# Performance work log

Hardware: AMD Instinct MI355X
Metric: run time of the kernel (lower is better)

The kernel has to match this reference:

```python
import jax, jax.numpy as jnp
import numpy as np

D = 2048      # d_hidden
F = 1408      # d_expert (routed)
E = 8         # n_routed_experts
K = 2         # n_experts_per_token
FS = 2816     # shared expert width = d_expert * n_shared_experts
B, S = 2, 1024


def setup_inputs() -> dict:
    key = jax.random.key(0)
    ks = jax.random.split(key, 9)
    sc = 0.02
    return {
        "x": jax.random.normal(ks[0], (B, S, D), dtype=jnp.float32),
        "Wr": jax.random.normal(ks[1], (E, D), dtype=jnp.float32) * sc,   # router Linear(d_hidden, E).weight
        "Wg": jax.random.normal(ks[2], (E, F, D), dtype=jnp.float32) * sc,  # per-expert W_gate.weight [F,D]
        "Wu": jax.random.normal(ks[3], (E, F, D), dtype=jnp.float32) * sc,  # per-expert W_up.weight
        "Wd": jax.random.normal(ks[4], (E, D, F), dtype=jnp.float32) * sc,  # per-expert W_down.weight [D,F]
        "Wsg": jax.random.normal(ks[5], (FS, D), dtype=jnp.float32) * sc,   # shared expert W_gate
        "Wsu": jax.random.normal(ks[6], (FS, D), dtype=jnp.float32) * sc,   # shared expert W_up
        "Wsd": jax.random.normal(ks[7], (D, FS), dtype=jnp.float32) * sc,   # shared expert W_down
    }


def reference(x, Wr, Wg, Wu, Wd, Wsg, Wsu, Wsd):
    silu = jax.nn.silu

    # Shared expert: SwiGLU FFN over all tokens
    sg = silu(jnp.einsum("bsd,fd->bsf", x, Wsg))
    su = jnp.einsum("bsd,fd->bsf", x, Wsu)
    shared_out = jnp.einsum("bsf,df->bsd", sg * su, Wsd)

    # Gating: softmax over expert logits, then top-k (sum-combine is order-invariant)
    logits = jnp.einsum("bsd,ed->bse", x, Wr)
    scores = jax.nn.softmax(logits, axis=-1)
    topk_scores, topk_idx = jax.lax.top_k(scores, K)            # [B,S,K]
    # Dense combine weights [B,S,E]: topk score where selected, else 0
    w_full = jnp.sum(jax.nn.one_hot(topk_idx, E, dtype=x.dtype) * topk_scores[..., None], axis=-2)

    # Routed experts (dense-over-experts equivalent of sorted grouped-GEMM dispatch)
    g = silu(jnp.einsum("bsd,efd->bsef", x, Wg))                # [B,S,E,F]
    u = jnp.einsum("bsd,efd->bsef", x, Wu)
    out_e = jnp.einsum("bsef,edf->bsed", g * u, Wd)             # [B,S,E,D]
    routed_out = jnp.einsum("bsed,bse->bsd", out_e, w_full)

    return routed_out + shared_out
```

## Files before the change

kernel.cpp:

```cpp
#include <hip/hip_runtime.h>
#include <hip/hip_bf16.h>

#define D_HID 2048
#define F_EXP 1408
#define E_NUM 8
#define FS_SH 2816
#define T_TOK 2048

#define O_WSG 0
#define O_WSU 5767168
#define O_WG  11534336
#define O_WU  34603008
#define O_WSD 57671680
#define O_WD  63438848
#define W_TOT 86507520

#define MAXT 24
#define GU_SH_BLK 176
#define DN_SH_BLK 128

typedef __attribute__((ext_vector_type(8))) short bf16x8;
typedef __attribute__((ext_vector_type(4))) float f32x4;
typedef __attribute__((ext_vector_type(4))) unsigned short u16x4;

#define AS1 __attribute__((address_space(1)))
#define AS3 __attribute__((address_space(3)))

__device__ __forceinline__ unsigned short f2bf(float f){
  unsigned u = __float_as_uint(f);
  u += 0x7fffu + ((u >> 16) & 1u);
  return (unsigned short)(u >> 16);
}

__global__ void convert_x_kernel(const float* __restrict__ x, unsigned short* __restrict__ xb){
  const int i = blockIdx.x * blockDim.x + threadIdx.x;
  float4 v = ((const float4*)x)[i];
  u16x4 h;
  h[0]=f2bf(v.x); h[1]=f2bf(v.y); h[2]=f2bf(v.z); h[3]=f2bf(v.w);
  ((u16x4*)xb)[i] = h;
}

__global__ __launch_bounds__(256) void convert_w_kernel(
    const float* __restrict__ Wsg, const float* __restrict__ Wsu,
    const float* __restrict__ Wg,  const float* __restrict__ Wu,
    const float* __restrict__ Wsd, const float* __restrict__ Wd,
    unsigned short* __restrict__ dst)
{
  const long e0 = ((long)blockIdx.x * 256 + threadIdx.x) * 8;
  const float* src; long lo;
  if      (e0 < (long)O_WSU){ src = Wsg; lo = e0 - O_WSG; }
  else if (e0 < (long)O_WG ){ src = Wsu; lo = e0 - O_WSU; }
  else if (e0 < (long)O_WU ){ src = Wg;  lo = e0 - O_WG;  }
  else if (e0 < (long)O_WSD){ src = Wu;  lo = e0 - O_WU;  }
  else if (e0 < (long)O_WD ){ src = Wsd; lo = e0 - O_WSD; }
  else                      { src = Wd;  lo = e0 - O_WD;  }
  const float4 a = ((const float4*)(src + lo))[0];
  const float4 b = ((const float4*)(src + lo))[1];
  u16x4 h0, h1;
  h0[0]=f2bf(a.x); h0[1]=f2bf(a.y); h0[2]=f2bf(a.z); h0[3]=f2bf(a.w);
  h1[0]=f2bf(b.x); h1[1]=f2bf(b.y); h1[2]=f2bf(b.z); h1[3]=f2bf(b.w);
  ((u16x4*)(dst + e0))[0] = h0;
  ((u16x4*)(dst + e0))[1] = h1;
}

__global__ __launch_bounds__(64) void router_kernel(const float* __restrict__ x,
                                                    const float* __restrict__ Wr,
                                                    int* __restrict__ topk_e,
                                                    float* __restrict__ topk_w){
  const int t = blockIdx.x;
  const int lane = threadIdx.x;
  const float* xt = x + (size_t)t * D_HID;
  float acc[E_NUM];
  #pragma unroll
  for (int e=0;e<E_NUM;e++) acc[e]=0.f;
  for (int d=lane; d<D_HID; d+=64){
    const float xv = xt[d];
    #pragma unroll
    for (int e=0;e<E_NUM;e++) acc[e] += xv * Wr[e*D_HID + d];
  }
  #pragma unroll
  for (int e=0;e<E_NUM;e++){
    #pragma unroll
    for (int off=32; off>0; off>>=1) acc[e] += __shfl_xor(acc[e], off);
  }
  if (lane==0){
    float m = acc[0];
    #pragma unroll
    for (int e=1;e<E_NUM;e++) m = fmaxf(m, acc[e]);
    float p[E_NUM]; float s = 0.f;
    #pragma unroll
    for (int e=0;e<E_NUM;e++){ p[e] = expf(acc[e]-m); s += p[e]; }
    const float inv = 1.f/s;
    int i0=0; float b0=p[0];
    #pragma unroll
    for (int e=1;e<E_NUM;e++) if (p[e] > b0){ b0=p[e]; i0=e; }
    int i1=-1; float b1=-1.f;
    #pragma unroll
    for (int e=0;e<E_NUM;e++) if (e!=i0 && p[e] > b1){ b1=p[e]; i1=e; }
    topk_e[t*2+0]=i0; topk_e[t*2+1]=i1;
    topk_w[t*2+0]=b0*inv; topk_w[t*2+1]=b1*inv;
  }
}

__global__ __launch_bounds__(1024) void build_lists_kernel(
    const int* __restrict__ topk_e, const float* __restrict__ topk_w,
    int* __restrict__ cnt, int* __restrict__ offs,
    int* __restrict__ assign_token, float* __restrict__ assign_w,
    int* __restrict__ token_slot,
    int* __restrict__ tile_rowbase, int* __restrict__ tile_e,
    int* __restrict__ tile_valid, int* __restrict__ n_rt)
{
  const int tid  = threadIdx.x;
  const int lane = tid & 63;
  const int wv   = tid >> 6;
  __shared__ int wsum[E_NUM][16];
  __shared__ int tot_s[E_NUM];
  __shared__ int offs_s[E_NUM];

  int   e_loc[4];
  float w_loc[4];
  #pragma unroll
  for (int j=0;j<4;j++){ e_loc[j]=topk_e[tid*4+j]; w_loc[j]=topk_w[tid*4+j]; }

  int c[E_NUM];
  #pragma unroll
  for (int e=0;e<E_NUM;e++){
    int s = 0;
    #pragma unroll
    for (int j=0;j<4;j++) s += (e_loc[j]==e) ? 1 : 0;
    c[e] = s;
  }
  int pre[E_NUM];
  #pragma unroll
  for (int e=0;e<E_NUM;e++){
    int v = c[e];
    #pragma unroll
    for (int off=1; off<64; off<<=1){
      int t = __shfl_up(v, off);
      if (lane >= off) v += t;
    }
    if (lane==63) wsum[e][wv] = v;
    pre[e] = v - c[e];
  }
  __syncthreads();
  if (tid < E_NUM){
    int s = 0;
    #pragma unroll
    for (int w=0; w<16; w++){ int t = wsum[tid][w]; wsum[tid][w] = s; s += t; }
    tot_s[tid] = s;
    cnt[tid]   = s;
  }
  __syncthreads();
  if (tid == 0){
    int s = 0;
    #pragma unroll
    for (int e=0;e<E_NUM;e++){ offs_s[e] = s; offs[e] = s; s += tot_s[e]; }
    int ntl = 0;
    for (int e=0;e<E_NUM;e++){
      for (int r=0; r<tot_s[e]; r+=256){
        tile_rowbase[ntl] = offs_s[e] + r;
        tile_e[ntl]       = e;
        int v = tot_s[e] - r; if (v > 256) v = 256;
        tile_valid[ntl]   = v;
        ntl++;
      }
    }
    n_rt[0] = ntl;
    for (int i=ntl;i<MAXT;i++){ tile_rowbase[i]=0; tile_e[i]=0; tile_valid[i]=0; }
  }
  __syncthreads();
  int local[E_NUM];
  #pragma unroll
  for (int e=0;e<E_NUM;e++) local[e]=0;
  #pragma unroll
  for (int j=0;j<4;j++){
    const int e = e_loc[j];
    int pos = 0;
    #pragma unroll
    for (int ee=0; ee<E_NUM; ee++)
      if (e == ee) pos = offs_s[ee] + wsum[ee][wv] + pre[ee] + local[ee];
    #pragma unroll
    for (int ee=0; ee<E_NUM; ee++) local[ee] += (e == ee) ? 1 : 0;
    const int entry = tid*4 + j;
    assign_token[pos] = entry >> 1;
    assign_w[pos]     = w_loc[j];
    token_slot[entry] = pos;
  }
}

__global__ __launch_bounds__(512,1) void gateup_fused(
    const unsigned short* __restrict__ xb,
    const unsigned short* __restrict__ wb,
    unsigned short* __restrict__ h_shared,
    unsigned short* __restrict__ h_routed,
    const int* __restrict__ tile_rowbase, const int* __restrict__ tile_e,
    const int* __restrict__ tile_valid, const int* __restrict__ n_rt,
    const int* __restrict__ assign_token)
{
  __shared__ __align__(16) char As[2][256*128];
  __shared__ __align__(16) char Bg[2][128*128];
  __shared__ __align__(16) char Bu[2][128*128];

  const int tid  = threadIdx.x;
  const int lane = tid & 63;
  const int wave = tid >> 6;
  const int wr = wave >> 1;
  const int wc = wave & 1;
  const int b = blockIdx.x;

  int nt, rowbase, valid, gather;
  const unsigned short *wg_base, *wu_base;
  unsigned short* H; int N;
  if (b < GU_SH_BLK){
    nt = b >> 3; const int mtile = b & 7;
    rowbase = mtile*256; valid = 256; gather = 0;
    wg_base = wb + O_WSG + (size_t)(nt*128) * D_HID;
    wu_base = wb + O_WSU + (size_t)(nt*128) * D_HID;
    H = h_shared; N = FS_SH;
  } else {
    const int rb = b - GU_SH_BLK;
    const int tile = rb % MAXT;
    nt = rb / MAXT;
    if (tile >= n_rt[0]) return;
    rowbase = tile_rowbase[tile];
    valid   = tile_valid[tile];
    const int e = tile_e[tile];
    gather = 1;
    wg_base = wb + O_WG + ((size_t)e*F_EXP + nt*128) * D_HID;
    wu_base = wb + O_WU + ((size_t)e*F_EXP + nt*128) * D_HID;
    H = h_routed; N = F_EXP;
  }

  f32x4 accg[4][4], accu[4][4];
  const f32x4 z = {0.f,0.f,0.f,0.f};
  #pragma unroll
  for (int m=0;m<4;m++)
    #pragma unroll
    for (int n=0;n<4;n++){ accg[m][n]=z; accu[m][n]=z; }

  const char* asrc[4];
  const int rowmax = rowbase + valid - 1;
  const int srccol = ((lane&7)<<4) ^ ((lane>>3)<<4);
  #pragma unroll
  for (int p=0;p<4;p++){
    const int row = wave*32 + p*8 + (lane>>3);
    int idx = rowbase + row;
    if (idx > rowmax) idx = rowmax;
    const size_t grow = gather ? (size_t)assign_token[idx] : (size_t)idx;
    asrc[p] = (const char*)(xb + grow * (size_t)D_HID) + srccol;
  }
  const int brow0 = wave*16 + (lane>>3);
  const char* gsrc = (const char*)(wg_base + (size_t)brow0 * D_HID) + srccol;
  const char* usrc = (const char*)(wu_base + (size_t)brow0 * D_HID) + srccol;
  const int pstrB = 8 * D_HID * 2;

  auto stage = [&](int bi, int kt){
    #pragma unroll
    for (int p=0;p<4;p++){
      __builtin_amdgcn_global_load_lds(
        (const AS1 void*)(asrc[p] + kt*128),
        (AS3 void*)(&As[bi][(wave*4 + p)*1024]), 16, 0, 0);
    }
    #pragma unroll
    for (int p=0;p<2;p++){
      __builtin_amdgcn_global_load_lds(
        (const AS1 void*)(gsrc + p*pstrB + kt*128),
        (AS3 void*)(&Bg[bi][(wave*2 + p)*1024]), 16, 0, 0);
      __builtin_amdgcn_global_load_lds(
        (const AS1 void*)(usrc + p*pstrB + kt*128),
        (AS3 void*)(&Bu[bi][(wave*2 + p)*1024]), 16, 0, 0);
    }
  };

  const int nK = D_HID / 64;
  stage(0, 0);
  int cur = 0;
  for (int kt = 0; kt < nK; ++kt){
    if (kt + 1 < nK){
      stage(cur^1, kt+1);
      asm volatile("s_waitcnt vmcnt(8)\n\ts_barrier" ::: "memory");
    } else {
      asm volatile("s_waitcnt vmcnt(0)\n\ts_barrier" ::: "memory");
    }
    #pragma unroll
    for (int kk=0;kk<2;kk++){
      const int kb = kk*64 + ((lane >> 4) << 4);
      bf16x8 a[4], bg[4], bu[4];
      #pragma unroll
      for (int m=0;m<4;m++){
        const int r = wr*64 + m*16 + (lane & 15);
        a[m] = *(const bf16x8*)(&As[cur][r*128 + (kb ^ ((r & 7) << 4))]);
      }
      #pragma unroll
      for (int n=0;n<4;n++){
        const int r = wc*64 + n*16 + (lane & 15);
        const int ofs = r*128 + (kb ^ ((r & 7) << 4));
        bg[n] = *(const bf16x8*)(&Bg[cur][ofs]);
        bu[n] = *(const bf16x8*)(&Bu[cur][ofs]);
      }
      #pragma unroll
      for (int m=0;m<4;m++)
        #pragma unroll
        for (int n=0;n<4;n++){
          accg[m][n] = __builtin_amdgcn_mfma_f32_16x16x32_bf16(a[m], bg[n], accg[m][n], 0,0,0);
          accu[m][n] = __builtin_amdgcn_mfma_f32_16x16x32_bf16(a[m], bu[n], accu[m][n], 0,0,0);
        }
    }
    asm volatile("s_barrier" ::: "memory");
    cur ^= 1;
  }

  const int colbase = nt*128 + wc*64;
  #pragma unroll
  for (int m=0;m<4;m++){
    #pragma unroll
    for (int r=0;r<4;r++){
      const int rr = wr*64 + m*16 + ((lane >> 4) << 2) + r;
      if (rr < valid){
        unsigned short* orow = H + (size_t)(rowbase + rr) * N;
        #pragma unroll
        for (int n=0;n<4;n++){
          const int col = colbase + n*16 + (lane & 15);
          const float g = accg[m][n][r];
          const float u = accu[m][n][r];
          const float h = (g / (1.f + __expf(-g))) * u;
          orow[col] = f2bf(h);
        }
      }
    }
  }
}

__global__ __launch_bounds__(512,1) void down_fused(
    const unsigned short* __restrict__ h_shared,
    const unsigned short* __restrict__ h_routed,
    const unsigned short* __restrict__ wb,
    float* __restrict__ out, float* __restrict__ y_routed,
    const int* __restrict__ tile_rowbase, const int* __restrict__ tile_e,
    const int* __restrict__ tile_valid, const int* __restrict__ n_rt,
    const float* __restrict__ assign_w)
{
  __shared__ __align__(16) char As[2][256*128];
  __shared__ __align__(16) char Bs[2][128*128];

  const int tid  = threadIdx.x;
  const int lane = tid & 63;
  const int wave = tid >> 6;
  const int wr = wave >> 1, wc = wave & 1;
  const int b = blockIdx.x;

  int nt, rowbase, valid, weighted, K;
  const unsigned short *A, *w_base;
  float* Out;
  if (b < DN_SH_BLK){
    nt = b >> 3; const int mtile = b & 7;
    rowbase = mtile*256; valid = 256; weighted = 0;
    A = h_shared; K = FS_SH;
    w_base = wb + O_WSD + (size_t)(nt*128) * FS_SH;
    Out = out;
  } else {
    const int rb = b - DN_SH_BLK;
    const int tile = rb % MAXT;
    nt = rb / MAXT;
    if (tile >= n_rt[0]) return;
    rowbase = tile_rowbase[tile];
    valid   = tile_valid[tile];
    const int e = tile_e[tile];
    weighted = 1;
    A = h_routed; K = F_EXP;
    w_base = wb + O_WD + ((size_t)e*D_HID + nt*128) * F_EXP;
    Out = y_routed;
  }
  const size_t K2 = (size_t)K * 2;

  f32x4 acc[4][4];
  const f32x4 z = {0.f,0.f,0.f,0.f};
  #pragma unroll
  for (int m=0;m<4;m++)
    #pragma unroll
    for (int n=0;n<4;n++) acc[m][n]=z;

  const char* asrc[4];
  const int rowmax = rowbase + valid - 1;
  const int srccol = ((lane&7)<<4) ^ ((lane>>3)<<4);
  #pragma unroll
  for (int p=0;p<4;p++){
    const int row = wave*32 + p*8 + (lane>>3);
    int idx = rowbase + row;
    if (idx > rowmax) idx = rowmax;
    asrc[p] = (const char*)A + (size_t)idx * K2 + srccol;
  }
  const int brow0 = wave*16 + (lane>>3);
  const char* bsrc = (const char*)w_base + (size_t)brow0 * K2 + srccol;
  const size_t pstrB = 8 * K2;

  auto stage = [&](int bi, int kt){
    #pragma unroll
    for (int p=0;p<4;p++){
      __builtin_amdgcn_global_load_lds(
        (const AS1 void*)(asrc[p] + kt*128),
        (AS3 void*)(&As[bi][(wave*4 + p)*1024]), 16, 0, 0);
    }
    #pragma unroll
    for (int p=0;p<2;p++){
      __builtin_amdgcn_global_load_lds(
        (const AS1 void*)(bsrc + p*pstrB + kt*128),
        (AS3 void*)(&Bs[bi][(wave*2 + p)*1024]), 16, 0, 0);
    }
  };

  const int nK = K / 64;
  stage(0, 0);
  int cur = 0;
  for (int kt = 0; kt < nK; ++kt){
    if (kt + 1 < nK){
      stage(cur^1, kt+1);
      asm volatile("s_waitcnt vmcnt(6)\n\ts_barrier" ::: "memory");
    } else {
      asm volatile("s_waitcnt vmcnt(0)\n\ts_barrier" ::: "memory");
    }
    #pragma unroll
    for (int kk=0;kk<2;kk++){
      const int kb = kk*64 + ((lane >> 4) << 4);
      bf16x8 a[4], bb[4];
      #pragma unroll
      for (int m=0;m<4;m++){
        const int r = wr*64 + m*16 + (lane & 15);
        a[m] = *(const bf16x8*)(&As[cur][r*128 + (kb ^ ((r & 7) << 4))]);
      }
      #pragma unroll
      for (int n=0;n<4;n++){
        const int r = wc*64 + n*16 + (lane & 15);
        bb[n] = *(const bf16x8*)(&Bs[cur][r*128 + (kb ^ ((r & 7) << 4))]);
      }
      #pragma unroll
      for (int m=0;m<4;m++)
        #pragma unroll
        for (int n=0;n<4;n++)
          acc[m][n] = __builtin_amdgcn_mfma_f32_16x16x32_bf16(a[m], bb[n], acc[m][n], 0,0,0);
    }
    asm volatile("s_barrier" ::: "memory");
    cur ^= 1;
  }

  const int colbase = nt*128 + wc*64;
  #pragma unroll
  for (int m=0;m<4;m++){
    #pragma unroll
    for (int r=0;r<4;r++){
      const int rr = wr*64 + m*16 + ((lane >> 4) << 2) + r;
      if (rr < valid){
        float w = 1.f;
        if (weighted) w = assign_w[rowbase + rr];
        float* orow = Out + (size_t)(rowbase + rr) * D_HID;
        #pragma unroll
        for (int n=0;n<4;n++){
          const int col = colbase + n*16 + (lane & 15);
          orow[col] = acc[m][n][r] * w;
        }
      }
    }
  }
}

__global__ void combine_kernel(float* __restrict__ out, const float* __restrict__ y,
                               const int* __restrict__ token_slot){
  const int i  = blockIdx.x * blockDim.x + threadIdx.x;
  const int t  = i >> 9;
  const int r4 = i & 511;
  const int s0 = token_slot[t*2+0];
  const int s1 = token_slot[t*2+1];
  const float4 a = ((const float4*)(y + (size_t)s0 * D_HID))[r4];
  const float4 b = ((const float4*)(y + (size_t)s1 * D_HID))[r4];
  float4 o = ((float4*)out)[i];
  o.x += a.x + b.x; o.y += a.y + b.y; o.z += a.z + b.z; o.w += a.w + b.w;
  ((float4*)out)[i] = o;
}

extern "C" void kernel_launch(void* const* d_in, const int* in_sizes, int n_in,
                              void* d_out, int out_size, void* d_ws, size_t ws_size,
                              hipStream_t stream){
  const float* x   = (const float*)d_in[0];
  const float* Wr  = (const float*)d_in[1];
  const float* Wg  = (const float*)d_in[2];
  const float* Wu  = (const float*)d_in[3];
  const float* Wd  = (const float*)d_in[4];
  const float* Wsg = (const float*)d_in[5];
  const float* Wsu = (const float*)d_in[6];
  const float* Wsd = (const float*)d_in[7];
  float* out = (float*)d_out;
  (void)in_sizes; (void)n_in; (void)out_size; (void)ws_size;

  char* ws = (char*)d_ws;
  size_t off = 0;
  auto alloc = [&](size_t bytes)->char*{
    char* p = ws + off; off += (bytes + 255) & ~(size_t)255; return p;
  };

  unsigned short* wb       = (unsigned short*)alloc((size_t)W_TOT * 2);
  unsigned short* xb       = (unsigned short*)alloc((size_t)T_TOK * D_HID * 2);
  unsigned short* h_shared = (unsigned short*)alloc((size_t)T_TOK * FS_SH * 2);
  unsigned short* h_routed = (unsigned short*)alloc((size_t)T_TOK * 2 * F_EXP * 2);
  float*          y_routed = (float*)alloc((size_t)T_TOK * 2 * D_HID * 4);
  int*   topk_e       = (int*)alloc(T_TOK*2*sizeof(int));
  float* topk_w       = (float*)alloc(T_TOK*2*sizeof(float));
  int*   cnt          = (int*)alloc(E_NUM*sizeof(int));
  int*   offs         = (int*)alloc(E_NUM*sizeof(int));
  int*   assign_token = (int*)alloc(T_TOK*2*sizeof(int));
  float* assign_w     = (float*)alloc(T_TOK*2*sizeof(float));
  int*   token_slot   = (int*)alloc(T_TOK*2*sizeof(int));
  int*   tile_rowbase = (int*)alloc(MAXT*sizeof(int));
  int*   tile_e       = (int*)alloc(MAXT*sizeof(int));
  int*   tile_valid   = (int*)alloc(MAXT*sizeof(int));
  int*   n_rt         = (int*)alloc(sizeof(int));

  convert_x_kernel<<<(T_TOK*D_HID/4)/256, 256, 0, stream>>>(x, xb);
  router_kernel<<<T_TOK, 64, 0, stream>>>(x, Wr, topk_e, topk_w);
  build_lists_kernel<<<1, 1024, 0, stream>>>(topk_e, topk_w, cnt, offs,
      assign_token, assign_w, token_slot, tile_rowbase, tile_e, tile_valid, n_rt);
  convert_w_kernel<<<W_TOT/8/256, 256, 0, stream>>>(Wsg, Wsu, Wg, Wu, Wsd, Wd, wb);

  gateup_fused<<<GU_SH_BLK + MAXT*(F_EXP/128), 512, 0, stream>>>(
      xb, wb, h_shared, h_routed, tile_rowbase, tile_e, tile_valid, n_rt, assign_token);
  down_fused<<<DN_SH_BLK + MAXT*(D_HID/128), 512, 0, stream>>>(
      h_shared, h_routed, wb, out, y_routed, tile_rowbase, tile_e, tile_valid, n_rt, assign_w);

  combine_kernel<<<(T_TOK*D_HID/4)/256, 256, 0, stream>>>(out, y_routed, token_slot);
}
```

Before: 387.2 us.

## Fuse down-weight conversion into gate/up kernel and restructure MFMA loop scheduling

The fp32-to-bf16 conversion of the down-projection weights (Wsd, Wd) moves out of the standalone conversion kernel and into the start of the gate/up GEMM kernel, spread across all its blocks. This is meant to overlap that memory-bound work with GEMM blocks instead of running it as a separate serial pass. The K-loop of both GEMM kernels is also rewritten into phases: LDS reads, then MFMA bursts under raised wave priority, with sched_barriers and extra s_barriers between phases, and the prefetch for the next stage issued after the first LDS reads. The trade-offs are more barriers per iteration and a full vmcnt(0) wait at the end of each iteration, which can cut the overlap between loads and compute. The fused conversion also lengthens the gate/up kernel, including blocks that would otherwise exit early.

```diff
diff --git a/kernel.cpp b/kernel.cpp
--- a/kernel.cpp
+++ b/kernel.cpp
@@ -17,6 +17,7 @@
 
 #define MAXT 24
 #define GU_SH_BLK 176
+#define GU_GRID   440
 #define DN_SH_BLK 128
 
 typedef __attribute__((ext_vector_type(8))) short bf16x8;
@@ -43,7 +44,6 @@
 __global__ __launch_bounds__(256) void convert_w_kernel(
     const float* __restrict__ Wsg, const float* __restrict__ Wsu,
     const float* __restrict__ Wg,  const float* __restrict__ Wu,
-    const float* __restrict__ Wsd, const float* __restrict__ Wd,
     unsigned short* __restrict__ dst)
 {
   const long e0 = ((long)blockIdx.x * 256 + threadIdx.x) * 8;
@@ -51,9 +51,7 @@
   if      (e0 < (long)O_WSU){ src = Wsg; lo = e0 - O_WSG; }
   else if (e0 < (long)O_WG ){ src = Wsu; lo = e0 - O_WSU; }
   else if (e0 < (long)O_WU ){ src = Wg;  lo = e0 - O_WG;  }
-  else if (e0 < (long)O_WSD){ src = Wu;  lo = e0 - O_WU;  }
-  else if (e0 < (long)O_WD ){ src = Wsd; lo = e0 - O_WSD; }
-  else                      { src = Wd;  lo = e0 - O_WD;  }
+  else                      { src = Wu;  lo = e0 - O_WU;  }
   const float4 a = ((const float4*)(src + lo))[0];
   const float4 b = ((const float4*)(src + lo))[1];
   u16x4 h0, h1;
@@ -190,7 +188,8 @@
 
 __global__ __launch_bounds__(512,1) void gateup_fused(
     const unsigned short* __restrict__ xb,
-    const unsigned short* __restrict__ wb,
+    unsigned short* __restrict__ wb,
+    const float* __restrict__ Wsd_f, const float* __restrict__ Wd_f,
     unsigned short* __restrict__ h_shared,
     unsigned short* __restrict__ h_routed,
     const int* __restrict__ tile_rowbase, const int* __restrict__ tile_e,
@@ -207,6 +206,22 @@
   const int wr = wave >> 1;
   const int wc = wave & 1;
   const int b = blockIdx.x;
+
+  {
+    const int nchunk = (W_TOT - O_WSD) / 8;
+    for (int i = b*512 + tid; i < nchunk; i += GU_GRID*512){
+      const long e0 = (long)O_WSD + (long)i * 8;
+      const float* src; long lo;
+      if (e0 < (long)O_WD){ src = Wsd_f; lo = e0 - O_WSD; } else { src = Wd_f; lo = e0 - O_WD; }
+      const float4 va = ((const float4*)(src + lo))[0];
+      const float4 vb = ((const float4*)(src + lo))[1];
+      u16x4 h0, h1;
+      h0[0]=f2bf(va.x); h0[1]=f2bf(va.y); h0[2]=f2bf(va.z); h0[3]=f2bf(va.w);
+      h1[0]=f2bf(vb.x); h1[1]=f2bf(vb.y); h1[2]=f2bf(vb.z); h1[3]=f2bf(vb.w);
+      ((u16x4*)(wb + e0))[0] = h0;
+      ((u16x4*)(wb + e0))[1] = h1;
+    }
+  }
 
   int nt, rowbase, valid, gather;
   const unsigned short *wg_base, *wu_base;
@@ -272,41 +287,105 @@
     }
   };
 
+  const int arow = wr*64 + (lane & 15);
+  const int brow = wc*64 + (lane & 15);
+  const int kq   = (lane >> 4) << 4;
+
   const int nK = D_HID / 64;
   stage(0, 0);
+  asm volatile("s_waitcnt vmcnt(0)\n\ts_barrier" ::: "memory");
   int cur = 0;
+  #pragma unroll 1
   for (int kt = 0; kt < nK; ++kt){
-    if (kt + 1 < nK){
-      stage(cur^1, kt+1);
-      asm volatile("s_waitcnt vmcnt(8)\n\ts_barrier" ::: "memory");
-    } else {
-      asm volatile("s_waitcnt vmcnt(0)\n\ts_barrier" ::: "memory");
-    }
-    #pragma unroll
-    for (int kk=0;kk<2;kk++){
-      const int kb = kk*64 + ((lane >> 4) << 4);
-      bf16x8 a[4], bg[4], bu[4];
+    bf16x8 a0[4], bx[4];
+    {
+      const int kb = 0*64 + kq;
       #pragma unroll
       for (int m=0;m<4;m++){
-        const int r = wr*64 + m*16 + (lane & 15);
-        a[m] = *(const bf16x8*)(&As[cur][r*128 + (kb ^ ((r & 7) << 4))]);
+        const int r = arow + m*16;
+        a0[m] = *(const bf16x8*)(&As[cur][r*128 + (kb ^ ((r & 7) << 4))]);
       }
       #pragma unroll
       for (int n=0;n<4;n++){
-        const int r = wc*64 + n*16 + (lane & 15);
-        const int ofs = r*128 + (kb ^ ((r & 7) << 4));
-        bg[n] = *(const bf16x8*)(&Bg[cur][ofs]);
-        bu[n] = *(const bf16x8*)(&Bu[cur][ofs]);
-      }
-      #pragma unroll
-      for (int m=0;m<4;m++)
-        #pragma unroll
-        for (int n=0;n<4;n++){
-          accg[m][n] = __builtin_amdgcn_mfma_f32_16x16x32_bf16(a[m], bg[n], accg[m][n], 0,0,0);
-          accu[m][n] = __builtin_amdgcn_mfma_f32_16x16x32_bf16(a[m], bu[n], accu[m][n], 0,0,0);
-        }
-    }
-    asm volatile("s_barrier" ::: "memory");
+        const int r = brow + n*16;
+        bx[n] = *(const bf16x8*)(&Bg[cur][r*128 + (kb ^ ((r & 7) << 4))]);
+      }
+    }
+    if (kt + 1 < nK) stage(cur^1, kt+1);
+    asm volatile("s_barrier" ::: "memory");
+    __builtin_amdgcn_sched_barrier(0);
+    __builtin_amdgcn_s_setprio(1);
+    #pragma unroll
+    for (int m=0;m<4;m++)
+      #pragma unroll
+      for (int n=0;n<4;n++)
+        accg[m][n] = __builtin_amdgcn_mfma_f32_16x16x32_bf16(a0[m], bx[n], accg[m][n], 0,0,0);
+    __builtin_amdgcn_s_setprio(0);
+    __builtin_amdgcn_sched_barrier(0);
+    asm volatile("s_barrier" ::: "memory");
+    {
+      const int kb = 0*64 + kq;
+      #pragma unroll
+      for (int n=0;n<4;n++){
+        const int r = brow + n*16;
+        bx[n] = *(const bf16x8*)(&Bu[cur][r*128 + (kb ^ ((r & 7) << 4))]);
+      }
+    }
+    asm volatile("s_barrier" ::: "memory");
+    __builtin_amdgcn_sched_barrier(0);
+    __builtin_amdgcn_s_setprio(1);
+    #pragma unroll
+    for (int m=0;m<4;m++)
+      #pragma unroll
+      for (int n=0;n<4;n++)
+        accu[m][n] = __builtin_amdgcn_mfma_f32_16x16x32_bf16(a0[m], bx[n], accu[m][n], 0,0,0);
+    __builtin_amdgcn_s_setprio(0);
+    __builtin_amdgcn_sched_barrier(0);
+    asm volatile("s_barrier" ::: "memory");
+    bf16x8 a1[4];
+    {
+      const int kb = 1*64 + kq;
+      #pragma unroll
+      for (int m=0;m<4;m++){
+        const int r = arow + m*16;
+        a1[m] = *(const bf16x8*)(&As[cur][r*128 + (kb ^ ((r & 7) << 4))]);
+      }
+      #pragma unroll
+      for (int n=0;n<4;n++){
+        const int r = brow + n*16;
+        bx[n] = *(const bf16x8*)(&Bg[cur][r*128 + (kb ^ ((r & 7) << 4))]);
+      }
+    }
+    asm volatile("s_barrier" ::: "memory");
+    __builtin_amdgcn_sched_barrier(0);
+    __builtin_amdgcn_s_setprio(1);
+    #pragma unroll
+    for (int m=0;m<4;m++)
+      #pragma unroll
+      for (int n=0;n<4;n++)
+        accg[m][n] = __builtin_amdgcn_mfma_f32_16x16x32_bf16(a1[m], bx[n], accg[m][n], 0,0,0);
+    __builtin_amdgcn_s_setprio(0);
+    __builtin_amdgcn_sched_barrier(0);
+    asm volatile("s_barrier" ::: "memory");
+    {
+      const int kb = 1*64 + kq;
+      #pragma unroll
+      for (int n=0;n<4;n++){
+        const int r = brow + n*16;
+        bx[n] = *(const bf16x8*)(&Bu[cur][r*128 + (kb ^ ((r & 7) << 4))]);
+      }
+    }
+    asm volatile("s_barrier" ::: "memory");
+    __builtin_amdgcn_sched_barrier(0);
+    __builtin_amdgcn_s_setprio(1);
+    #pragma unroll
+    for (int m=0;m<4;m++)
+      #pragma unroll
+      for (int n=0;n<4;n++)
+        accu[m][n] = __builtin_amdgcn_mfma_f32_16x16x32_bf16(a1[m], bx[n], accu[m][n], 0,0,0);
+    __builtin_amdgcn_s_setprio(0);
+    __builtin_amdgcn_sched_barrier(0);
+    asm volatile("s_waitcnt vmcnt(0)\n\ts_barrier" ::: "memory");
     cur ^= 1;
   }
 
@@ -409,37 +488,66 @@
     }
   };
 
+  const int arow = wr*64 + (lane & 15);
+  const int brow = wc*64 + (lane & 15);
+  const int kq   = (lane >> 4) << 4;
+
   const int nK = K / 64;
   stage(0, 0);
+  asm volatile("s_waitcnt vmcnt(0)\n\ts_barrier" ::: "memory");
   int cur = 0;
+  #pragma unroll 1
   for (int kt = 0; kt < nK; ++kt){
-    if (kt + 1 < nK){
-      stage(cur^1, kt+1);
-      asm volatile("s_waitcnt vmcnt(6)\n\ts_barrier" ::: "memory");
-    } else {
-      asm volatile("s_waitcnt vmcnt(0)\n\ts_barrier" ::: "memory");
-    }
-    #pragma unroll
-    for (int kk=0;kk<2;kk++){
-      const int kb = kk*64 + ((lane >> 4) << 4);
-      bf16x8 a[4], bb[4];
+    bf16x8 a[4], bb[4];
+    {
+      const int kb = 0*64 + kq;
       #pragma unroll
       for (int m=0;m<4;m++){
-        const int r = wr*64 + m*16 + (lane & 15);
+        const int r = arow + m*16;
         a[m] = *(const bf16x8*)(&As[cur][r*128 + (kb ^ ((r & 7) << 4))]);
       }
       #pragma unroll
       for (int n=0;n<4;n++){
-        const int r = wc*64 + n*16 + (lane & 15);
+        const int r = brow + n*16;
         bb[n] = *(const bf16x8*)(&Bs[cur][r*128 + (kb ^ ((r & 7) << 4))]);
       }
-      #pragma unroll
-      for (int m=0;m<4;m++)
-        #pragma unroll
-        for (int n=0;n<4;n++)
-          acc[m][n] = __builtin_amdgcn_mfma_f32_16x16x32_bf16(a[m], bb[n], acc[m][n], 0,0,0);
-    }
-    asm volatile("s_barrier" ::: "memory");
+    }
+    if (kt + 1 < nK) stage(cur^1, kt+1);
+    asm volatile("s_barrier" ::: "memory");
+    __builtin_amdgcn_sched_barrier(0);
+    __builtin_amdgcn_s_setprio(1);
+    #pragma unroll
+    for (int m=0;m<4;m++)
+      #pragma unroll
+      for (int n=0;n<4;n++)
+        acc[m][n] = __builtin_amdgcn_mfma_f32_16x16x32_bf16(a[m], bb[n], acc[m][n], 0,0,0);
+    __builtin_amdgcn_s_setprio(0);
+    __builtin_amdgcn_sched_barrier(0);
+    asm volatile("s_barrier" ::: "memory");
+    {
+      const int kb = 1*64 + kq;
+      #pragma unroll
+      for (int m=0;m<4;m++){
+        const int r = arow + m*16;
+        a[m] = *(const bf16x8*)(&As[cur][r*128 + (kb ^ ((r & 7) << 4))]);
+      }
+      #pragma unroll
+      for (int n=0;n<4;n++){
+        const int r = brow + n*16;
+        bb[n] = *(const bf16x8*)(&Bs[cur][r*128 + (kb ^ ((r & 7) << 4))]);
+      }
+    }
+    asm volatile("s_barrier" ::: "memory");
+    __builtin_amdgcn_sched_barrier(0);
+    __builtin_amdgcn_s_setprio(1);
+    #pragma unroll
+    for (int m=0;m<4;m++)
+      #pragma unroll
+      for (int n=0;n<4;n++)
+        acc[m][n] = __builtin_amdgcn_mfma_f32_16x16x32_bf16(a[m], bb[n], acc[m][n], 0,0,0);
+    __builtin_amdgcn_s_setprio(0);
+    __builtin_amdgcn_sched_barrier(0);
+    asm volatile("s_waitcnt vmcnt(0)\n\ts_barrier" ::: "memory");
     cur ^= 1;
   }
 
@@ -518,10 +626,10 @@
   router_kernel<<<T_TOK, 64, 0, stream>>>(x, Wr, topk_e, topk_w);
   build_lists_kernel<<<1, 1024, 0, stream>>>(topk_e, topk_w, cnt, offs,
       assign_token, assign_w, token_slot, tile_rowbase, tile_e, tile_valid, n_rt);
-  convert_w_kernel<<<W_TOT/8/256, 256, 0, stream>>>(Wsg, Wsu, Wg, Wu, Wsd, Wd, wb);
-
-  gateup_fused<<<GU_SH_BLK + MAXT*(F_EXP/128), 512, 0, stream>>>(
-      xb, wb, h_shared, h_routed, tile_rowbase, tile_e, tile_valid, n_rt, assign_token);
+  convert_w_kernel<<<O_WSD/8/256, 256, 0, stream>>>(Wsg, Wsu, Wg, Wu, wb);
+
+  gateup_fused<<<GU_GRID, 512, 0, stream>>>(
+      xb, wb, Wsd, Wd, h_shared, h_routed, tile_rowbase, tile_e, tile_valid, n_rt, assign_token);
   down_fused<<<DN_SH_BLK + MAXT*(D_HID/128), 512, 0, stream>>>(
       h_shared, h_routed, wb, out, y_routed, tile_rowbase, tile_e, tile_valid, n_rt, assign_w);
 
```

Measured after the change: 396.6 us. +2.4%, slower.

## Overlap down-proj weight conversion with gate/up GEMM and fuse x conversion into router

Applied to the files above, without the earlier changes.

Moves the fp32-to-bf16 conversion of the down-projection weights out of the standalone convert kernel. Extra blocks appended to the gate/up GEMM grid now do it, so the conversion runs alongside the GEMM. The x-to-bf16 conversion is folded into the router kernel, which now uses float4 loads, removing one launch and one read of x. Both GEMMs also remap block indices to interleave tiles across XCDs. The trade-off is that conversion blocks compete with GEMM blocks for CUs and bandwidth.

```diff
diff --git a/kernel.cpp b/kernel.cpp
--- a/kernel.cpp
+++ b/kernel.cpp
@@ -17,6 +17,9 @@
 
 #define MAXT 24
 #define GU_SH_BLK 176
+#define GU_GEMM   440
+#define GU_CONV   64
+#define DN_GRID   512
 #define DN_SH_BLK 128
 
 typedef __attribute__((ext_vector_type(8))) short bf16x8;
@@ -32,18 +35,9 @@
   return (unsigned short)(u >> 16);
 }
 
-__global__ void convert_x_kernel(const float* __restrict__ x, unsigned short* __restrict__ xb){
-  const int i = blockIdx.x * blockDim.x + threadIdx.x;
-  float4 v = ((const float4*)x)[i];
-  u16x4 h;
-  h[0]=f2bf(v.x); h[1]=f2bf(v.y); h[2]=f2bf(v.z); h[3]=f2bf(v.w);
-  ((u16x4*)xb)[i] = h;
-}
-
 __global__ __launch_bounds__(256) void convert_w_kernel(
     const float* __restrict__ Wsg, const float* __restrict__ Wsu,
     const float* __restrict__ Wg,  const float* __restrict__ Wu,
-    const float* __restrict__ Wsd, const float* __restrict__ Wd,
     unsigned short* __restrict__ dst)
 {
   const long e0 = ((long)blockIdx.x * 256 + threadIdx.x) * 8;
@@ -51,9 +45,7 @@
   if      (e0 < (long)O_WSU){ src = Wsg; lo = e0 - O_WSG; }
   else if (e0 < (long)O_WG ){ src = Wsu; lo = e0 - O_WSU; }
   else if (e0 < (long)O_WU ){ src = Wg;  lo = e0 - O_WG;  }
-  else if (e0 < (long)O_WSD){ src = Wu;  lo = e0 - O_WU;  }
-  else if (e0 < (long)O_WD ){ src = Wsd; lo = e0 - O_WSD; }
-  else                      { src = Wd;  lo = e0 - O_WD;  }
+  else                      { src = Wu;  lo = e0 - O_WU;  }
   const float4 a = ((const float4*)(src + lo))[0];
   const float4 b = ((const float4*)(src + lo))[1];
   u16x4 h0, h1;
@@ -65,18 +57,28 @@
 
 __global__ __launch_bounds__(64) void router_kernel(const float* __restrict__ x,
                                                     const float* __restrict__ Wr,
+                                                    unsigned short* __restrict__ xb,
                                                     int* __restrict__ topk_e,
                                                     float* __restrict__ topk_w){
   const int t = blockIdx.x;
   const int lane = threadIdx.x;
   const float* xt = x + (size_t)t * D_HID;
+  unsigned short* xbt = xb + (size_t)t * D_HID;
   float acc[E_NUM];
   #pragma unroll
   for (int e=0;e<E_NUM;e++) acc[e]=0.f;
-  for (int d=lane; d<D_HID; d+=64){
-    const float xv = xt[d];
-    #pragma unroll
-    for (int e=0;e<E_NUM;e++) acc[e] += xv * Wr[e*D_HID + d];
+  #pragma unroll
+  for (int j=0;j<8;j++){
+    const int d = j*256 + lane*4;
+    const float4 v = *(const float4*)(xt + d);
+    u16x4 h;
+    h[0]=f2bf(v.x); h[1]=f2bf(v.y); h[2]=f2bf(v.z); h[3]=f2bf(v.w);
+    *(u16x4*)(xbt + d) = h;
+    #pragma unroll
+    for (int e=0;e<E_NUM;e++){
+      const float4 w = *(const float4*)(Wr + e*D_HID + d);
+      acc[e] += v.x*w.x + v.y*w.y + v.z*w.z + v.w*w.w;
+    }
   }
   #pragma unroll
   for (int e=0;e<E_NUM;e++){
@@ -190,7 +192,8 @@
 
 __global__ __launch_bounds__(512,1) void gateup_fused(
     const unsigned short* __restrict__ xb,
-    const unsigned short* __restrict__ wb,
+    unsigned short* __restrict__ wb,
+    const float* __restrict__ Wsd_f, const float* __restrict__ Wd_f,
     unsigned short* __restrict__ h_shared,
     unsigned short* __restrict__ h_routed,
     const int* __restrict__ tile_rowbase, const int* __restrict__ tile_e,
@@ -202,11 +205,32 @@
   __shared__ __align__(16) char Bu[2][128*128];
 
   const int tid  = threadIdx.x;
+  const int braw = blockIdx.x;
+
+  if (braw >= GU_GEMM){
+    const int cb = braw - GU_GEMM;
+    const long nchunk = (long)(W_TOT - O_WSD) / 8;
+    for (long i = (long)cb*512 + tid; i < nchunk; i += (long)GU_CONV*512){
+      const long e0 = (long)O_WSD + i * 8;
+      const float* src; long lo;
+      if (e0 < (long)O_WD){ src = Wsd_f; lo = e0 - O_WSD; } else { src = Wd_f; lo = e0 - O_WD; }
+      const float4 va = ((const float4*)(src + lo))[0];
+      const float4 vb = ((const float4*)(src + lo))[1];
+      u16x4 h0, h1;
+      h0[0]=f2bf(va.x); h0[1]=f2bf(va.y); h0[2]=f2bf(va.z); h0[3]=f2bf(va.w);
+      h1[0]=f2bf(vb.x); h1[1]=f2bf(vb.y); h1[2]=f2bf(vb.z); h1[3]=f2bf(vb.w);
+      ((u16x4*)(wb + e0))[0] = h0;
+      ((u16x4*)(wb + e0))[1] = h1;
+    }
+    return;
+  }
+
+  const int b = (braw % 8) * (GU_GEMM/8) + braw / 8;
+
   const int lane = tid & 63;
   const int wave = tid >> 6;
   const int wr = wave >> 1;
   const int wc = wave & 1;
-  const int b = blockIdx.x;
 
   int nt, rowbase, valid, gather;
   const unsigned short *wg_base, *wu_base;
@@ -344,10 +368,11 @@
   __shared__ __align__(16) char Bs[2][128*128];
 
   const int tid  = threadIdx.x;
+  const int braw = blockIdx.x;
+  const int b = (braw % 8) * (DN_GRID/8) + braw / 8;
   const int lane = tid & 63;
   const int wave = tid >> 6;
   const int wr = wave >> 1, wc = wave & 1;
-  const int b = blockIdx.x;
 
   int nt, rowbase, valid, weighted, K;
   const unsigned short *A, *w_base;
@@ -514,15 +539,14 @@
   int*   tile_valid   = (int*)alloc(MAXT*sizeof(int));
   int*   n_rt         = (int*)alloc(sizeof(int));
 
-  convert_x_kernel<<<(T_TOK*D_HID/4)/256, 256, 0, stream>>>(x, xb);
-  router_kernel<<<T_TOK, 64, 0, stream>>>(x, Wr, topk_e, topk_w);
+  router_kernel<<<T_TOK, 64, 0, stream>>>(x, Wr, xb, topk_e, topk_w);
   build_lists_kernel<<<1, 1024, 0, stream>>>(topk_e, topk_w, cnt, offs,
       assign_token, assign_w, token_slot, tile_rowbase, tile_e, tile_valid, n_rt);
-  convert_w_kernel<<<W_TOT/8/256, 256, 0, stream>>>(Wsg, Wsu, Wg, Wu, Wsd, Wd, wb);
-
-  gateup_fused<<<GU_SH_BLK + MAXT*(F_EXP/128), 512, 0, stream>>>(
-      xb, wb, h_shared, h_routed, tile_rowbase, tile_e, tile_valid, n_rt, assign_token);
-  down_fused<<<DN_SH_BLK + MAXT*(D_HID/128), 512, 0, stream>>>(
+  convert_w_kernel<<<O_WSD/8/256, 256, 0, stream>>>(Wsg, Wsu, Wg, Wu, wb);
+
+  gateup_fused<<<GU_GEMM + GU_CONV, 512, 0, stream>>>(
+      xb, wb, Wsd, Wd, h_shared, h_routed, tile_rowbase, tile_e, tile_valid, n_rt, assign_token);
+  down_fused<<<DN_GRID, 512, 0, stream>>>(
       h_shared, h_routed, wb, out, y_routed, tile_rowbase, tile_e, tile_valid, n_rt, assign_w);
 
   combine_kernel<<<(T_TOK*D_HID/4)/256, 256, 0, stream>>>(out, y_routed, token_slot);
```

New measurement: 388.1 us. About the same (+0.2%).
